# Performance work log

Measured on AMD Instinct MI355X. Metric: run time of the kernel, lower is better.

## Reference

```python
import jax, jax.numpy as jnp
import numpy as np

N_NODES = 100000
D = 128
E_ER = 800000
E_EE = 800000
E_RR = 400000


def setup_inputs() -> dict:
    key = jax.random.key(0)
    ks = jax.random.split(key, 16)
    def lin(kw, kb, out_d, in_d):
        s = 1.0 / np.sqrt(in_d)
        w = jax.random.uniform(kw, (out_d, in_d), minval=-s, maxval=s, dtype=jnp.float32)
        b = jax.random.uniform(kb, (out_d,), minval=-s, maxval=s, dtype=jnp.float32)
        return w, b
    W_attn_w, W_attn_b = lin(ks[0], ks[1], D, 2 * D)
    w0_w, w0_b = lin(ks[2], ks[3], 1, D)
    W1_w, W1_b = lin(ks[4], ks[5], D, D)
    W2_w, W2_b = lin(ks[6], ks[7], D, D)
    W3_w, W3_b = lin(ks[8], ks[9], D, D)
    return {
        "node_emb": jax.random.normal(ks[10], (N_NODES, D), dtype=jnp.float32),
        "er_src": jax.random.randint(ks[11], (E_ER,), 0, N_NODES),
        "er_dst": jax.random.randint(ks[12], (E_ER,), 0, N_NODES),
        "ee_src": jax.random.randint(ks[13], (E_EE,), 0, N_NODES),
        "ee_dst": jax.random.randint(ks[14], (E_EE,), 0, N_NODES),
        "ee_weight": jax.random.uniform(ks[15], (E_EE,), dtype=jnp.float32),
        "rr_src": jax.random.randint(jax.random.fold_in(key, 100), (E_RR,), 0, N_NODES),
        "rr_dst": jax.random.randint(jax.random.fold_in(key, 101), (E_RR,), 0, N_NODES),
        "W_attn_w": W_attn_w, "W_attn_b": W_attn_b,
        "w0_w": w0_w, "w0_b": w0_b,
        "W1_w": W1_w, "W1_b": W1_b,
        "W2_w": W2_w, "W2_b": W2_b,
        "W3_w": W3_w, "W3_b": W3_b,
    }


def _segment_softmax(values, segment_ids, num_segments):
    # torch version: seg_max initialized to zeros with include_self=True -> max(0, seg max)
    seg_max = jnp.maximum(jax.ops.segment_max(values, segment_ids, num_segments=num_segments), 0.0)
    exp_v = jnp.exp(values - seg_max[segment_ids])
    seg_sum = jax.ops.segment_sum(exp_v, segment_ids, num_segments=num_segments)
    return exp_v / (seg_sum[segment_ids] + 1e-9)


def reference(node_emb, er_src, er_dst, ee_src, ee_dst, ee_weight, rr_src, rr_dst,
              W_attn_w, W_attn_b, w0_w, w0_b, W1_w, W1_b, W2_w, W2_b, W3_w, W3_b):
    N = node_emb.shape[0]
    # --- attention aggregation over er edges (entity <- relation) ---
    h_emb = node_emb[er_src]            # (E, D)
    r_emb = node_emb[er_dst]            # (E, D)
    pair = jnp.concatenate([r_emb, h_emb], axis=-1)  # (E, 2D)
    e_ij = (jnp.tanh(pair @ W_attn_w.T + W_attn_b) @ w0_w.T + w0_b)[:, 0]  # (E,)
    attn = _segment_softmax(e_ij, er_src, N)
    attn_agg = jax.ops.segment_sum(attn[:, None] * r_emb, er_src, num_segments=N)
    # --- mean aggregation ---
    mean_agg = jax.ops.segment_sum(h_emb, er_dst, num_segments=N)
    mean_cnt = jax.ops.segment_sum(jnp.ones_like(er_dst, dtype=node_emb.dtype), er_dst, num_segments=N)
    w = ee_weight[:, None]
    mean_agg = mean_agg + jax.ops.segment_sum(w * node_emb[ee_dst], ee_src, num_segments=N)
    mean_cnt = mean_cnt + jax.ops.segment_sum(ee_weight, ee_src, num_segments=N)
    mean_agg = mean_agg + jax.ops.segment_sum(node_emb[rr_dst], rr_src, num_segments=N)
    mean_cnt = mean_cnt + jax.ops.segment_sum(jnp.ones_like(rr_src, dtype=node_emb.dtype), rr_src, num_segments=N)
    mean_agg = mean_agg / jnp.clip(mean_cnt, 1.0, None)[:, None]
    return (jnp.tanh(node_emb @ W1_w.T + W1_b)
            + jnp.tanh(attn_agg @ W2_w.T + W2_b)
            + jnp.tanh(mean_agg @ W3_w.T + W3_b))
```

## Files before the change

### kernel.cpp

```cpp
#include <hip/hip_runtime.h>

typedef unsigned int u32;
typedef unsigned short u16;

#define D 128

typedef __attribute__((ext_vector_type(8))) short bf16x8;
typedef __attribute__((ext_vector_type(4))) float f32x4;
#define MFMA16x16(a, b, c) __builtin_amdgcn_mfma_f32_16x16x32_bf16(a, b, c, 0, 0, 0)

__device__ inline float b2f(u32 h) { return __uint_as_float((h & 0xffffu) << 16); }
__device__ inline u16 f2b(float f) {
    u32 u = __float_as_uint(f);
    return (u16)((u + 0x7fffu + ((u >> 16) & 1u)) >> 16);
}
__device__ inline float tanh_fast(float x) {
    x = fminf(fmaxf(x, -15.f), 15.f);
    float e = __expf(2.f * x);
    return (e - 1.f) * __builtin_amdgcn_rcpf(e + 1.f);
}


__global__ __launch_bounds__(256) void k_bhist(const int* __restrict__ er_src,
                                               const int* __restrict__ er_dst,
                                               const int* __restrict__ ee_src,
                                               const int* __restrict__ rr_src,
                                               int* __restrict__ histA,
                                               int* __restrict__ histM,
                                               int E_ER, int E_EE, int E_RR, int NBK) {
    __shared__ int hA[1024], hM[1024];
    int tid = threadIdx.x;
    for (int j = tid; j < NBK; j += 256) { hA[j] = 0; hM[j] = 0; }
    __syncthreads();
    int E_T = 2 * E_ER + E_EE + E_RR;
    int stride = gridDim.x * 256;
    for (int e = blockIdx.x * 256 + tid; e < E_T; e += stride) {
        int i = e;
        if (i < E_ER) { atomicAdd(&hA[er_src[i] >> 7], 1); continue; }
        i -= E_ER;
        int key;
        if (i < E_ER) key = er_dst[i];
        else {
            i -= E_ER;
            key = (i < E_EE) ? ee_src[i] : rr_src[i - E_EE];
        }
        atomicAdd(&hM[key >> 7], 1);
    }
    __syncthreads();
    for (int j = tid; j < NBK; j += 256) {
        histA[j * 256 + blockIdx.x] = hA[j];
        histM[j * 256 + blockIdx.x] = hM[j];
    }
}

__global__ void k_scan1_dual(const int* __restrict__ cnt2, int n,
                             int* __restrict__ off_src, int* __restrict__ off_mean,
                             int* __restrict__ bsum, int nbs) {
    __shared__ int sh[256];
    int b = blockIdx.x;
    const int* cnt = cnt2;
    int* out = off_src;
    int* bs = bsum;
    if (b >= nbs) { b -= nbs; cnt = cnt2 + n; out = off_mean; bs = bsum + 256; }
    int t = threadIdx.x;
    int base = b * 1024 + t * 4;
    int v0 = (base < n) ? cnt[base] : 0;
    int v1 = (base + 1 < n) ? cnt[base + 1] : 0;
    int v2 = (base + 2 < n) ? cnt[base + 2] : 0;
    int v3 = (base + 3 < n) ? cnt[base + 3] : 0;
    int s4 = v0 + v1 + v2 + v3;
    sh[t] = s4;
    __syncthreads();
    for (int o = 1; o < 256; o <<= 1) {
        int x = (t >= o) ? sh[t - o] : 0;
        __syncthreads();
        sh[t] += x;
        __syncthreads();
    }
    int p = sh[t] - s4;
    if (t == 255) bs[b] = sh[255];
    if (base < n) out[base] = p;
    p += v0;
    if (base + 1 < n) out[base + 1] = p;
    p += v1;
    if (base + 2 < n) out[base + 2] = p;
    p += v2;
    if (base + 3 < n) out[base + 3] = p;
}

__global__ void k_scan2_dual(int* __restrict__ bsum, int nb,
                             int* __restrict__ totA, int* __restrict__ totB) {
    __shared__ int sh[256];
    int* bs = bsum + blockIdx.x * 256;
    int* tot = blockIdx.x ? totB : totA;
    int t = threadIdx.x;
    int v = (t < nb) ? bs[t] : 0;
    sh[t] = v;
    __syncthreads();
    for (int o = 1; o < 256; o <<= 1) {
        int x = (t >= o) ? sh[t - o] : 0;
        __syncthreads();
        sh[t] += x;
        __syncthreads();
    }
    if (t < nb) bs[t] = sh[t] - v;
    if (t == 255) *tot = sh[255];
}

__global__ void k_scan3b(int* __restrict__ offA, int* __restrict__ offM,
                         const int* __restrict__ bsum, int n) {
    int i = blockIdx.x * 256 + threadIdx.x;
    if (i < n) offA[i] += bsum[i >> 10];
    else if (i < 2 * n) offM[i - n] += bsum[256 + ((i - n) >> 10)];
}

__global__ __launch_bounds__(256) void k_bin(const int* __restrict__ er_src,
                                             const int* __restrict__ er_dst,
                                             const int* __restrict__ ee_src,
                                             const int* __restrict__ ee_dst,
                                             const int* __restrict__ rr_src,
                                             const int* __restrict__ rr_dst,
                                             const float* __restrict__ ee_w,
                                             const int* __restrict__ offA,
                                             const int* __restrict__ offM,
                                             int* __restrict__ recA,
                                             int2* __restrict__ recM,
                                             int E_ER, int E_EE, int E_RR, int NBK) {
    __shared__ int cA[1024], cM[1024];
    int tid = threadIdx.x, blk = blockIdx.x;
    for (int j = tid; j < NBK; j += 256) {
        cA[j] = offA[j * 256 + blk];
        cM[j] = offM[j * 256 + blk];
    }
    __syncthreads();
    int E_T = 2 * E_ER + E_EE + E_RR;
    int stride = gridDim.x * 256;
    for (int e = blk * 256 + tid; e < E_T; e += stride) {
        int i = e;
        if (i < E_ER) {
            int key = er_src[i];
            int p = atomicAdd(&cA[key >> 7], 1);
            recA[p] = er_dst[i] | ((key & 127) << 17);
            continue;
        }
        i -= E_ER;
        int sct, gat;
        float w;
        if (i < E_ER) {
            sct = er_dst[i]; gat = er_src[i]; w = 1.f;
        } else {
            i -= E_ER;
            if (i < E_EE) { sct = ee_src[i]; gat = ee_dst[i]; w = ee_w[i]; }
            else { i -= E_EE; sct = rr_src[i]; gat = rr_dst[i]; w = 1.f; }
        }
        int p = atomicAdd(&cM[sct >> 7], 1);
        recM[p] = make_int2(gat | ((sct & 127) << 17), __float_as_int(w));
    }
}

__global__ __launch_bounds__(256) void k_bucket(const int* __restrict__ offA_h,
                                                const int* __restrict__ offM_h,
                                                const int* __restrict__ recA,
                                                const int2* __restrict__ recM,
                                                int* __restrict__ off_src,
                                                int* __restrict__ off_mean,
                                                int* __restrict__ er_lst,
                                                int2* __restrict__ gpack,
                                                int E_ER, int E_M, int N, int NBK) {
    __shared__ int cnt[256];
    __shared__ int scanbuf[256];
    __shared__ int cur[256];
    int b = blockIdx.x, tid = threadIdx.x;
    int a0 = offA_h[b * 256];
    int a1 = (b + 1 < NBK) ? offA_h[(b + 1) * 256] : E_ER;
    int m0 = offM_h[b * 256];
    int m1 = (b + 1 < NBK) ? offM_h[(b + 1) * 256] : E_M;
    cnt[tid] = 0;
    __syncthreads();
    for (int i = a0 + tid; i < a1; i += 256) atomicAdd(&cnt[(recA[i] >> 17) & 127], 1);
    for (int i = m0 + tid; i < m1; i += 256) atomicAdd(&cnt[128 + ((recM[i].x >> 17) & 127)], 1);
    __syncthreads();
    int v = cnt[tid];
    scanbuf[tid] = v;
    __syncthreads();
    for (int o = 1; o < 128; o <<= 1) {
        int x = ((tid & 127) >= o) ? scanbuf[tid - o] : 0;
        __syncthreads();
        scanbuf[tid] += x;
        __syncthreads();
    }
    int excl = scanbuf[tid] - v;
    int pos = ((tid < 128) ? a0 : m0) + excl;
    cur[tid] = pos;
    int node = b * 128 + (tid & 127);
    if (node < N) {
        if (tid < 128) off_src[node] = pos;
        else off_mean[node] = pos;
    }
    if (b == 0 && tid == 0) { off_src[N] = E_ER; off_mean[N] = E_M; }
    __syncthreads();
    for (int i = a0 + tid; i < a1; i += 256) {
        int r = recA[i];
        int p = atomicAdd(&cur[(r >> 17) & 127], 1);
        er_lst[p] = r & 0x1FFFF;
    }
    for (int i = m0 + tid; i < m1; i += 256) {
        int2 r = recM[i];
        int p = atomicAdd(&cur[128 + ((r.x >> 17) & 127)], 1);
        gpack[p] = make_int2(r.x & 0x1FFFF, r.y);
    }
}

__global__ void k_cast4(const float* __restrict__ src, u16* __restrict__ dst, int n4) {
    int i = blockIdx.x * 256 + threadIdx.x;
    if (i >= n4) return;
    float4 v = ((const float4*)src)[i];
    ushort4 o;
    o.x = f2b(v.x); o.y = f2b(v.y); o.z = f2b(v.z); o.w = f2b(v.w);
    ((ushort4*)dst)[i] = o;
}

__global__ void k_cast_w(const float* __restrict__ Wattn,
                         const float* __restrict__ W1, const float* __restrict__ W2,
                         const float* __restrict__ W3,
                         u16* __restrict__ Wcat, u16* __restrict__ W123h) {
    int i = blockIdx.x * 256 + threadIdx.x;
    if (i < 32768) {
        int dd = i >> 7, k = i & 127;
        float v = (dd < 128) ? Wattn[(size_t)dd * 256 + k]
                             : Wattn[(size_t)(dd - 128) * 256 + 128 + k];
        Wcat[i] = f2b(v);
        return;
    }
    i -= 32768;
    if (i < 16384) { W123h[i] = f2b(W1[i]); return; }
    i -= 16384;
    if (i < 16384) { W123h[16384 + i] = f2b(W2[i]); return; }
    i -= 16384;
    if (i < 16384) W123h[32768 + i] = f2b(W3[i]);
}

__global__ __launch_bounds__(256) void k_precompute_mfma(const u16* __restrict__ embh,
                                                         const u16* __restrict__ Wcat,
                                                         u16* __restrict__ A, int N) {
    __shared__ u16 sX[64][136];
    int nb = blockIdx.x * 64;
    int tid = threadIdx.x;
    for (int i = tid; i < 1024; i += 256) {
        int row = i >> 4, c8 = i & 15;
        int n = nb + row;
        uint4 v = make_uint4(0u, 0u, 0u, 0u);
        if (n < N) v = *(const uint4*)(embh + (size_t)n * 128 + c8 * 8);
        *(uint4*)&sX[row][c8 * 8] = v;
    }
    __syncthreads();
    int wid = tid >> 6, lane = tid & 63;
    int quad = lane >> 4, l15 = lane & 15;
#pragma unroll
    for (int ns = 0; ns < 4; ns++) {
        int dbase = (wid * 4 + ns) * 16;
        bf16x8 b[4];
#pragma unroll
        for (int ks = 0; ks < 4; ks++)
            b[ks] = *(const bf16x8*)(Wcat + (size_t)(dbase + l15) * 128 + ks * 32 + quad * 8);
#pragma unroll
        for (int ms = 0; ms < 4; ms++) {
            f32x4 acc = {0.f, 0.f, 0.f, 0.f};
#pragma unroll
            for (int ks = 0; ks < 4; ks++) {
                bf16x8 a = *(const bf16x8*)&sX[ms * 16 + l15][ks * 32 + quad * 8];
                acc = MFMA16x16(a, b[ks], acc);
            }
#pragma unroll
            for (int r = 0; r < 4; r++) {
                int row = nb + ms * 16 + quad * 4 + r;
                if (row < N) A[(size_t)row * 256 + dbase + l15] = f2b(acc[r]);
            }
        }
    }
}

__global__ __launch_bounds__(512) void k_fuse(const u16* __restrict__ A,
                                              const int* __restrict__ offA,
                                              const int* __restrict__ lstA,
                                              const int* __restrict__ offM,
                                              const int2* __restrict__ gpack,
                                              const u16* __restrict__ embh,
                                              const float* __restrict__ Wb,
                                              const float* __restrict__ w0w,
                                              const float* __restrict__ w0b,
                                              const u16* __restrict__ W123h,
                                              const float* __restrict__ b1,
                                              const float* __restrict__ b2,
                                              const float* __restrict__ b3,
                                              float* __restrict__ out, int N) {
    __shared__ u16 sX[3][64][136];
    int nb = blockIdx.x * 64;
    int tid = threadIdx.x;
    int wid = tid >> 6, lane = tid & 63;
    int quad = lane >> 4, l15 = lane & 15;

    for (int j = tid; j < 1024; j += 512) {
        int row = j >> 4, c8 = j & 15;
        int n = nb + row;
        uint4 v = make_uint4(0u, 0u, 0u, 0u);
        if (n < N) v = *(const uint4*)(embh + (size_t)n * 128 + c8 * 8);
        *(uint4*)&sX[0][row][c8 * 8] = v;
    }

    float wwv[8], bbv[8];
#pragma unroll
    for (int j = 0; j < 8; j++) {
        wwv[j] = w0w[l15 * 8 + j];
        bbv[j] = Wb[l15 * 8 + j];
    }
    float w0bias = w0b[0];

    for (int i = 0; i < 8; ++i) {
        int local = wid * 8 + i;
        int node = nb + local;
        if (node < N) {
            bf16x8 ah8 = *(const bf16x8*)(A + (size_t)node * 256 + 128 + l15 * 8);
            const u32* ahp = (const u32*)&ah8;
            float haxb[8];
#pragma unroll
            for (int j = 0; j < 4; j++) {
                haxb[2 * j]     = b2f(ahp[j]) + bbv[2 * j];
                haxb[2 * j + 1] = b2f(ahp[j] >> 16) + bbv[2 * j + 1];
            }
            int s0 = offA[node], s1 = offA[node + 1];
            float accx[8] = {0.f, 0.f, 0.f, 0.f, 0.f, 0.f, 0.f, 0.f};
            float lsum = 0.f;
            for (int s = s0; s < s1; s += 8) {
                int i0 = s + quad, i1 = s + 4 + quad;
                bool va = i0 < s1, vb = i1 < s1;
                int d0 = lstA[va ? i0 : s0];
                int d1 = lstA[vb ? i1 : s0];
                bf16x8 ar0 = *(const bf16x8*)(A + (size_t)d0 * 256 + l15 * 8);
                bf16x8 ar1 = *(const bf16x8*)(A + (size_t)d1 * 256 + l15 * 8);
                bf16x8 ev0 = *(const bf16x8*)(embh + (size_t)d0 * 128 + l15 * 8);
                bf16x8 ev1 = *(const bf16x8*)(embh + (size_t)d1 * 128 + l15 * 8);
                const u32* a0p = (const u32*)&ar0;
                const u32* a1p = (const u32*)&ar1;
                float p0 = 0.f, p1 = 0.f;
#pragma unroll
                for (int j = 0; j < 4; j++) {
                    p0 += tanh_fast(b2f(a0p[j]) + haxb[2 * j]) * wwv[2 * j] +
                          tanh_fast(b2f(a0p[j] >> 16) + haxb[2 * j + 1]) * wwv[2 * j + 1];
                    p1 += tanh_fast(b2f(a1p[j]) + haxb[2 * j]) * wwv[2 * j] +
                          tanh_fast(b2f(a1p[j] >> 16) + haxb[2 * j + 1]) * wwv[2 * j + 1];
                }
#pragma unroll
                for (int o = 1; o < 16; o <<= 1) {
                    p0 += __shfl_xor(p0, o);
                    p1 += __shfl_xor(p1, o);
                }
                float e0 = va ? __expf(p0 + w0bias) : 0.f;
                float e1 = vb ? __expf(p1 + w0bias) : 0.f;
                lsum += e0 + e1;
                const u32* e0p = (const u32*)&ev0;
                const u32* e1p = (const u32*)&ev1;
#pragma unroll
                for (int j = 0; j < 4; j++) {
                    accx[2 * j]     += e0 * b2f(e0p[j]) + e1 * b2f(e1p[j]);
                    accx[2 * j + 1] += e0 * b2f(e0p[j] >> 16) + e1 * b2f(e1p[j] >> 16);
                }
            }
#pragma unroll
            for (int j = 0; j < 8; j++) {
                accx[j] += __shfl_xor(accx[j], 16);
                accx[j] += __shfl_xor(accx[j], 32);
            }
            lsum += __shfl_xor(lsum, 16);
            lsum += __shfl_xor(lsum, 32);
            float inv = 1.f / (lsum + 1e-9f);
            if (quad == 0) {
                uint4 o4;
                u32* op = (u32*)&o4;
#pragma unroll
                for (int j = 0; j < 4; j++)
                    op[j] = (u32)f2b(accx[2 * j] * inv) |
                            ((u32)f2b(accx[2 * j + 1] * inv) << 16);
                *(uint4*)&sX[1][local][l15 * 8] = o4;
            }

            s0 = offM[node]; s1 = offM[node + 1];
            float accm[8] = {0.f, 0.f, 0.f, 0.f, 0.f, 0.f, 0.f, 0.f};
            float c = 0.f;
            for (int s = s0; s < s1; s += 8) {
                int i0 = s + quad, i1 = s + 4 + quad;
                bool va = i0 < s1, vb = i1 < s1;
                int2 pk0 = gpack[va ? i0 : s0];
                int2 pk1 = gpack[vb ? i1 : s0];
                float w0 = va ? __int_as_float(pk0.y) : 0.f;
                float w1 = vb ? __int_as_float(pk1.y) : 0.f;
                bf16x8 ev0 = *(const bf16x8*)(embh + (size_t)pk0.x * 128 + l15 * 8);
                bf16x8 ev1 = *(const bf16x8*)(embh + (size_t)pk1.x * 128 + l15 * 8);
                const u32* e0p = (const u32*)&ev0;
                const u32* e1p = (const u32*)&ev1;
#pragma unroll
                for (int j = 0; j < 4; j++) {
                    accm[2 * j]     += w0 * b2f(e0p[j]) + w1 * b2f(e1p[j]);
                    accm[2 * j + 1] += w0 * b2f(e0p[j] >> 16) + w1 * b2f(e1p[j] >> 16);
                }
                c += w0 + w1;
            }
#pragma unroll
            for (int j = 0; j < 8; j++) {
                accm[j] += __shfl_xor(accm[j], 16);
                accm[j] += __shfl_xor(accm[j], 32);
            }
            c += __shfl_xor(c, 16);
            c += __shfl_xor(c, 32);
            c = c > 1.f ? c : 1.f;
            float minv = 1.f / c;
            if (quad == 0) {
                uint4 o4;
                u32* op = (u32*)&o4;
#pragma unroll
                for (int j = 0; j < 4; j++)
                    op[j] = (u32)f2b(accm[2 * j] * minv) |
                            ((u32)f2b(accm[2 * j + 1] * minv) << 16);
                *(uint4*)&sX[2][local][l15 * 8] = o4;
            }
        }
    }
    __syncthreads();

    int d = wid * 16 + l15;
    const float* biases[3] = {b1, b2, b3};
    f32x4 res0 = {0.f, 0.f, 0.f, 0.f};
    f32x4 res1 = {0.f, 0.f, 0.f, 0.f};
    f32x4 res2 = {0.f, 0.f, 0.f, 0.f};
    f32x4 res3 = {0.f, 0.f, 0.f, 0.f};
#pragma unroll
    for (int arr = 0; arr < 3; arr++) {
        bf16x8 b[4];
#pragma unroll
        for (int ks = 0; ks < 4; ks++)
            b[ks] = *(const bf16x8*)(W123h + (size_t)arr * 16384 +
                                     (size_t)d * 128 + ks * 32 + quad * 8);
        float bias = biases[arr][d];
#pragma unroll
        for (int ms = 0; ms < 4; ms++) {
            f32x4 acc = {0.f, 0.f, 0.f, 0.f};
#pragma unroll
            for (int ks = 0; ks < 4; ks++) {
                bf16x8 a = *(const bf16x8*)&sX[arr][ms * 16 + l15][ks * 32 + quad * 8];
                acc = MFMA16x16(a, b[ks], acc);
            }
            f32x4& res = (ms == 0) ? res0 : (ms == 1) ? res1 : (ms == 2) ? res2 : res3;
#pragma unroll
            for (int r = 0; r < 4; r++)
                res[r] += tanh_fast(acc[r] + bias);
        }
    }
#pragma unroll
    for (int ms = 0; ms < 4; ms++) {
        f32x4& res = (ms == 0) ? res0 : (ms == 1) ? res1 : (ms == 2) ? res2 : res3;
#pragma unroll
        for (int r = 0; r < 4; r++) {
            int orow = nb + ms * 16 + quad * 4 + r;
            if (orow < N)
                out[(size_t)orow * 128 + d] = res[r];
        }
    }
}

extern "C" void kernel_launch(void* const* d_in, const int* in_sizes, int n_in,
                              void* d_out, int out_size, void* d_ws, size_t ws_size,
                              hipStream_t stream) {
    const float* emb     = (const float*)d_in[0];
    const int*   er_src  = (const int*)d_in[1];
    const int*   er_dst  = (const int*)d_in[2];
    const int*   ee_src  = (const int*)d_in[3];
    const int*   ee_dst  = (const int*)d_in[4];
    const float* ee_w    = (const float*)d_in[5];
    const int*   rr_src  = (const int*)d_in[6];
    const int*   rr_dst  = (const int*)d_in[7];
    const float* Wattn   = (const float*)d_in[8];
    const float* Wattn_b = (const float*)d_in[9];
    const float* w0w     = (const float*)d_in[10];
    const float* w0b     = (const float*)d_in[11];
    const float* W1      = (const float*)d_in[12];
    const float* b1      = (const float*)d_in[13];
    const float* W2      = (const float*)d_in[14];
    const float* b2      = (const float*)d_in[15];
    const float* W3      = (const float*)d_in[16];
    const float* b3      = (const float*)d_in[17];
    float* out = (float*)d_out;

    int N    = in_sizes[0] / D;
    int E_ER = in_sizes[1];
    int E_EE = in_sizes[3];
    int E_RR = in_sizes[6];
    int E_M  = E_ER + E_EE + E_RR;

    int NBK = (N + 127) >> 7;
    int HL  = NBK * 256;

    char* ws = (char*)d_ws;
    size_t off_b = 0;
    auto alloc = [&](size_t bytes) -> void* {
        void* p = ws + off_b;
        off_b += (bytes + 255) & ~(size_t)255;
        return p;
    };
    u16*   embh   = (u16*)alloc((size_t)N * 128 * 2);
    u16*   A      = (u16*)alloc((size_t)N * 256 * 2);
    u16*   Wcat_h = (u16*)alloc(256 * 128 * 2);
    u16*   W123h  = (u16*)alloc(3 * 128 * 128 * 2);
    int*   off_src  = (int*)alloc((size_t)(N + 1) * 4);
    int*   off_mean = (int*)alloc((size_t)(N + 1) * 4);
    int*   bsum     = (int*)alloc(514 * 4);
    int*   er_lst   = (int*)alloc((size_t)E_ER * 4);
    int2*  gpack    = (int2*)alloc((size_t)E_M * 8);

    char* Ab   = (char*)A;
    int2* recM = (int2*)Ab;
    int*  recA = (int*)(Ab + (size_t)E_M * 8);
    int*  hist2 = (int*)(Ab + (size_t)E_M * 8 + (size_t)E_ER * 4);
    int*  offHA = hist2 + 2 * HL;
    int*  offHM = offHA + HL;

    int nbh = (HL + 1023) / 1024;

    k_cast4<<<((N * 128 / 4) + 255) / 256, 256, 0, stream>>>(emb, embh, N * 128 / 4);
    k_cast_w<<<(81920 + 255) / 256, 256, 0, stream>>>(Wattn, W1, W2, W3, Wcat_h, W123h);

    k_bhist<<<256, 256, 0, stream>>>(er_src, er_dst, ee_src, rr_src,
                                     hist2, hist2 + HL, E_ER, E_EE, E_RR, NBK);
    k_scan1_dual<<<2 * nbh, 256, 0, stream>>>(hist2, HL, offHA, offHM, bsum, nbh);
    k_scan2_dual<<<2, 256, 0, stream>>>(bsum, nbh, bsum + 512, bsum + 513);
    k_scan3b<<<(2 * HL + 255) / 256, 256, 0, stream>>>(offHA, offHM, bsum, HL);
    k_bin<<<256, 256, 0, stream>>>(er_src, er_dst, ee_src, ee_dst, rr_src, rr_dst, ee_w,
                                   offHA, offHM, recA, recM, E_ER, E_EE, E_RR, NBK);
    k_bucket<<<NBK, 256, 0, stream>>>(offHA, offHM, recA, recM,
                                      off_src, off_mean, er_lst, gpack,
                                      E_ER, E_M, N, NBK);

    k_precompute_mfma<<<(N + 63) / 64, 256, 0, stream>>>(embh, Wcat_h, A, N);
    k_fuse<<<(N + 63) / 64, 512, 0, stream>>>(A, off_src, er_lst, off_mean, gpack,
                                              embh, Wattn_b, w0w, w0b, W123h,
                                              b1, b2, b3, out, N);
}
```

Before: 508.6 us.

## Interleave projected-r and bf16 embedding rows into one 512-byte record per node

```diff
diff --git a/kernel.cpp b/kernel.cpp
--- a/kernel.cpp
+++ b/kernel.cpp
@@ -19,6 +19,7 @@
     float e = __expf(2.f * x);
     return (e - 1.f) * __builtin_amdgcn_rcpf(e + 1.f);
 }
+
 
 
 __global__ __launch_bounds__(256) void k_bhist(const int* __restrict__ er_src,
@@ -211,13 +212,15 @@
     }
 }
 
-__global__ void k_cast4(const float* __restrict__ src, u16* __restrict__ dst, int n4) {
+__global__ void k_cast4(const float* __restrict__ src, u16* __restrict__ AE, int n4) {
     int i = blockIdx.x * 256 + threadIdx.x;
     if (i >= n4) return;
     float4 v = ((const float4*)src)[i];
     ushort4 o;
     o.x = f2b(v.x); o.y = f2b(v.y); o.z = f2b(v.z); o.w = f2b(v.w);
-    ((ushort4*)dst)[i] = o;
+    int base = i * 4;
+    int n = base >> 7, d = base & 127;
+    *(ushort4*)(AE + (size_t)n * 256 + 128 + d) = o;
 }
 
 __global__ void k_cast_w(const float* __restrict__ Wattn,
@@ -240,9 +243,9 @@
     if (i < 16384) W123h[32768 + i] = f2b(W3[i]);
 }
 
-__global__ __launch_bounds__(256) void k_precompute_mfma(const u16* __restrict__ embh,
-                                                         const u16* __restrict__ Wcat,
-                                                         u16* __restrict__ A, int N) {
+__global__ __launch_bounds__(256) void k_precompute_mfma(const u16* __restrict__ Wcat,
+                                                         u16* __restrict__ AE,
+                                                         u16* __restrict__ AH, int N) {
     __shared__ u16 sX[64][136];
     int nb = blockIdx.x * 64;
     int tid = threadIdx.x;
@@ -250,7 +253,7 @@
         int row = i >> 4, c8 = i & 15;
         int n = nb + row;
         uint4 v = make_uint4(0u, 0u, 0u, 0u);
-        if (n < N) v = *(const uint4*)(embh + (size_t)n * 128 + c8 * 8);
+        if (n < N) v = *(const uint4*)(AE + (size_t)n * 256 + 128 + c8 * 8);
         *(uint4*)&sX[row][c8 * 8] = v;
     }
     __syncthreads();
@@ -274,18 +277,23 @@
 #pragma unroll
             for (int r = 0; r < 4; r++) {
                 int row = nb + ms * 16 + quad * 4 + r;
-                if (row < N) A[(size_t)row * 256 + dbase + l15] = f2b(acc[r]);
-            }
-        }
-    }
-}
-
-__global__ __launch_bounds__(512) void k_fuse(const u16* __restrict__ A,
+                if (row < N) {
+                    if (dbase < 128)
+                        AE[(size_t)row * 256 + dbase + l15] = f2b(acc[r]);
+                    else
+                        AH[(size_t)row * 128 + (dbase - 128) + l15] = f2b(acc[r]);
+                }
+            }
+        }
+    }
+}
+
+__global__ __launch_bounds__(512) void k_fuse(const u16* __restrict__ AE,
+                                              const u16* __restrict__ AH,
                                               const int* __restrict__ offA,
                                               const int* __restrict__ lstA,
                                               const int* __restrict__ offM,
                                               const int2* __restrict__ gpack,
-                                              const u16* __restrict__ embh,
                                               const float* __restrict__ Wb,
                                               const float* __restrict__ w0w,
                                               const float* __restrict__ w0b,
@@ -304,7 +312,7 @@
         int row = j >> 4, c8 = j & 15;
         int n = nb + row;
         uint4 v = make_uint4(0u, 0u, 0u, 0u);
-        if (n < N) v = *(const uint4*)(embh + (size_t)n * 128 + c8 * 8);
+        if (n < N) v = *(const uint4*)(AE + (size_t)n * 256 + 128 + c8 * 8);
         *(uint4*)&sX[0][row][c8 * 8] = v;
     }
 
@@ -320,7 +328,7 @@
         int local = wid * 8 + i;
         int node = nb + local;
         if (node < N) {
-            bf16x8 ah8 = *(const bf16x8*)(A + (size_t)node * 256 + 128 + l15 * 8);
+            bf16x8 ah8 = *(const bf16x8*)(AH + (size_t)node * 128 + l15 * 8);
             const u32* ahp = (const u32*)&ah8;
             float haxb[8];
 #pragma unroll
@@ -336,10 +344,10 @@
                 bool va = i0 < s1, vb = i1 < s1;
                 int d0 = lstA[va ? i0 : s0];
                 int d1 = lstA[vb ? i1 : s0];
-                bf16x8 ar0 = *(const bf16x8*)(A + (size_t)d0 * 256 + l15 * 8);
-                bf16x8 ar1 = *(const bf16x8*)(A + (size_t)d1 * 256 + l15 * 8);
-                bf16x8 ev0 = *(const bf16x8*)(embh + (size_t)d0 * 128 + l15 * 8);
-                bf16x8 ev1 = *(const bf16x8*)(embh + (size_t)d1 * 128 + l15 * 8);
+                bf16x8 ar0 = *(const bf16x8*)(AE + (size_t)d0 * 256 + l15 * 8);
+                bf16x8 ar1 = *(const bf16x8*)(AE + (size_t)d1 * 256 + l15 * 8);
+                bf16x8 ev0 = *(const bf16x8*)(AE + (size_t)d0 * 256 + 128 + l15 * 8);
+                bf16x8 ev1 = *(const bf16x8*)(AE + (size_t)d1 * 256 + 128 + l15 * 8);
                 const u32* a0p = (const u32*)&ar0;
                 const u32* a1p = (const u32*)&ar1;
                 float p0 = 0.f, p1 = 0.f;
@@ -394,8 +402,8 @@
                 int2 pk1 = gpack[vb ? i1 : s0];
                 float w0 = va ? __int_as_float(pk0.y) : 0.f;
                 float w1 = vb ? __int_as_float(pk1.y) : 0.f;
-                bf16x8 ev0 = *(const bf16x8*)(embh + (size_t)pk0.x * 128 + l15 * 8);
-                bf16x8 ev1 = *(const bf16x8*)(embh + (size_t)pk1.x * 128 + l15 * 8);
+                bf16x8 ev0 = *(const bf16x8*)(AE + (size_t)pk0.x * 256 + 128 + l15 * 8);
+                bf16x8 ev1 = *(const bf16x8*)(AE + (size_t)pk1.x * 256 + 128 + l15 * 8);
                 const u32* e0p = (const u32*)&ev0;
                 const u32* e1p = (const u32*)&ev1;
 #pragma unroll
@@ -506,8 +514,8 @@
         off_b += (bytes + 255) & ~(size_t)255;
         return p;
     };
-    u16*   embh   = (u16*)alloc((size_t)N * 128 * 2);
-    u16*   A      = (u16*)alloc((size_t)N * 256 * 2);
+    u16*   AE     = (u16*)alloc((size_t)N * 256 * 2);
+    u16*   AH     = (u16*)alloc((size_t)N * 128 * 2);
     u16*   Wcat_h = (u16*)alloc(256 * 128 * 2);
     u16*   W123h  = (u16*)alloc(3 * 128 * 128 * 2);
     int*   off_src  = (int*)alloc((size_t)(N + 1) * 4);
@@ -515,17 +523,15 @@
     int*   bsum     = (int*)alloc(514 * 4);
     int*   er_lst   = (int*)alloc((size_t)E_ER * 4);
     int2*  gpack    = (int2*)alloc((size_t)E_M * 8);
-
-    char* Ab   = (char*)A;
-    int2* recM = (int2*)Ab;
-    int*  recA = (int*)(Ab + (size_t)E_M * 8);
-    int*  hist2 = (int*)(Ab + (size_t)E_M * 8 + (size_t)E_ER * 4);
-    int*  offHA = hist2 + 2 * HL;
-    int*  offHM = offHA + HL;
+    int2*  recM     = (int2*)alloc((size_t)E_M * 8);
+    int*   recA     = (int*)alloc((size_t)E_ER * 4);
+    int*   hist2    = (int*)alloc((size_t)2 * HL * 4);
+    int*   offHA    = (int*)alloc((size_t)HL * 4);
+    int*   offHM    = (int*)alloc((size_t)HL * 4);
 
     int nbh = (HL + 1023) / 1024;
 
-    k_cast4<<<((N * 128 / 4) + 255) / 256, 256, 0, stream>>>(emb, embh, N * 128 / 4);
+    k_cast4<<<((N * 128 / 4) + 255) / 256, 256, 0, stream>>>(emb, AE, N * 128 / 4);
     k_cast_w<<<(81920 + 255) / 256, 256, 0, stream>>>(Wattn, W1, W2, W3, Wcat_h, W123h);
 
     k_bhist<<<256, 256, 0, stream>>>(er_src, er_dst, ee_src, rr_src,
@@ -539,8 +545,8 @@
                                       off_src, off_mean, er_lst, gpack,
                                       E_ER, E_M, N, NBK);
 
-    k_precompute_mfma<<<(N + 63) / 64, 256, 0, stream>>>(embh, Wcat_h, A, N);
-    k_fuse<<<(N + 63) / 64, 512, 0, stream>>>(A, off_src, er_lst, off_mean, gpack,
-                                              embh, Wattn_b, w0w, w0b, W123h,
+    k_precompute_mfma<<<(N + 63) / 64, 256, 0, stream>>>(Wcat_h, AE, AH, N);
+    k_fuse<<<(N + 63) / 64, 512, 0, stream>>>(AE, AH, off_src, er_lst, off_mean, gpack,
+                                              Wattn_b, w0w, w0b, W123h,
                                               b1, b2, b3, out, N);
 }
```

Measured after the change: 516.4 us. Within noise of the previous version (+1.5%).
